# Kernel optimization log

Measured on AMD Instinct MI355X. Metric: run time of the kernel, lower is better.

Reference implementation:

```python
import jax, jax.numpy as jnp
import numpy as np

N = 512       # num_nodes (feature dim of x == num_nodes, per GCNConv(num_nodes, f1))
BZ = 32       # subjects
TC = 256      # tc_length
F1 = 256
F2 = 128
E = 524288    # edges in the given (corr) graph over all bz*N nodes
NTOT = BZ * N
SLOPE = 0.2   # leaky relu negative_slope


def setup_inputs() -> dict:
    key = jax.random.key(0)
    ks = jax.random.split(key, 17)
    w = lambda k, shape: (jax.random.normal(k, shape, jnp.float32) * (shape[-1] ** -0.5))
    return {
        "x": jax.random.normal(ks[0], (NTOT, N), jnp.float32),
        "t": jax.random.normal(ks[1], (NTOT, TC), jnp.float32),
        "gumbel_u": jax.random.uniform(ks[2], (BZ, N, N, 2), jnp.float32),
        "edge_index": jax.random.randint(ks[3], (2, E), 0, NTOT, jnp.int64 if jax.config.jax_enable_x64 else jnp.int32),
        "conv1_w": w(ks[4], (F1, N)),
        "conv1_b": jnp.zeros((F1,), jnp.float32),
        "conv2_w": w(ks[5], (F2, F1)),
        "conv2_b": jnp.zeros((F2,), jnp.float32),
        "fc_cat_w": w(ks[6], (2, 2 * TC)),
        "fc_cat_b": jnp.zeros((2,), jnp.float32),
        "fcn1_w": w(ks[7], (256, F2 * 2 * N)),
        "fcn1_b": jnp.zeros((256,), jnp.float32),
        "fcn2_w": w(ks[8], (32, 256)),
        "fcn2_b": jnp.zeros((32,), jnp.float32),
        "fcn3_w": w(ks[9], (2, 32)),
        "fcn3_b": jnp.zeros((2,), jnp.float32),
    }


def _gcn_dense(x, A, W, b):
    # PyG GCNConv on a dense 0/1 adjacency A (edge r->c means A[r,c]=1):
    # add self loop, in-degree symmetric norm, aggregate sources into targets.
    n = A.shape[0]
    Ah = A + jnp.eye(n, dtype=A.dtype)
    deg = Ah.sum(axis=0)                                  # in-degree (targets = cols)
    dis = jnp.where(deg > 0, jax.lax.rsqrt(deg), 0.0)
    M = dis[:, None] * Ah * dis[None, :]                  # M[j,i] = d_j^-1/2 A_hat[j,i] d_i^-1/2
    return M.T @ (x @ W.T) + b


def _gcn_sparse(x, row, col, W, b):
    n = x.shape[0]
    loops = jnp.arange(n, dtype=row.dtype)
    r = jnp.concatenate([row, loops])
    c = jnp.concatenate([col, loops])
    deg = jax.ops.segment_sum(jnp.ones_like(c, x.dtype), c, num_segments=n)
    dis = jnp.where(deg > 0, jax.lax.rsqrt(deg), 0.0)
    norm = dis[r] * dis[c]                                # [E+n]
    xw = x @ W.T                                          # [n, out]
    out = jax.ops.segment_sum(xw[r] * norm[:, None], c, num_segments=n)
    return out + b


def reference(x, t, gumbel_u, edge_index, conv1_w, conv1_b, conv2_w, conv2_b,
              fc_cat_w, fc_cat_b, fcn1_w, fcn1_b, fcn2_w, fcn2_b, fcn3_w, fcn3_b):
    bz = t.shape[0] // N
    tb = t.reshape(bz, N, -1)
    xb = x.reshape(bz, N, -1)
    # fc_cat(relu(cat([senders, receivers]))) factors into per-node terms:
    Ws = fc_cat_w[:, :TC]   # multiplies senders half
    Wr = fc_cat_w[:, TC:]   # multiplies receivers half

    def per_sample(ti, xi, ui):
        u = jax.nn.relu(ti)                               # [N, TC]
        ls = u @ Ws.T                                     # [N, 2] sender term
        lr = u @ Wr.T                                     # [N, 2] receiver term
        # pair k = i*N+j has receiver t_i, sender t_j
        logits = lr[:, None, :] + ls[None, :, :] + fc_cat_b   # [N, N, 2]
        g = -jnp.log(-jnp.log(jnp.clip(ui, 1e-9, 1.0 - 1e-9)))  # Gumbel(0,1)
        y = logits + g                                    # tau = 1
        A = (jnp.argmax(y, axis=-1) == 0).astype(xi.dtype)    # hard sample, class 0 => edge
        A = jax.lax.stop_gradient(A)                      # torch.where -> indices blocks grad
        h = jax.nn.relu(_gcn_dense(xi, A, conv1_w, conv1_b))
        return _gcn_dense(h, A, conv2_w, conv2_b)         # [N, F2]

    x_op = jax.vmap(per_sample)(tb, xb, gumbel_u)         # [bz, N, F2]

    row, col = edge_index[0], edge_index[1]
    x_corr = jax.nn.relu(_gcn_sparse(x, row, col, conv1_w, conv1_b))
    x_corr = _gcn_sparse(x_corr, row, col, conv2_w, conv2_b)   # [bz*N, F2]

    emb = jnp.concatenate([x_op.reshape(-1, F2), x_corr], axis=1)  # [bz*N, 2*F2]
    emb = emb.reshape(bz, -1)                             # [bz, 2*F2*N]
    h = jax.nn.leaky_relu(emb @ fcn1_w.T + fcn1_b, SLOPE)
    h = jax.nn.leaky_relu(h @ fcn2_w.T + fcn2_b, SLOPE)
    return h @ fcn3_w.T + fcn3_b                          # [bz, 2]
```

## Files before the change

kernel.cpp:

```cpp
#include <hip/hip_runtime.h>
#include <hip/hip_bf16.h>

typedef __bf16 bf16_t;
typedef __bf16 bf16x8 __attribute__((ext_vector_type(8)));
typedef __bf16 bf16x4 __attribute__((ext_vector_type(4)));
typedef float f32x4 __attribute__((ext_vector_type(4)));

constexpr int kN = 512;
constexpr int kBZ = 32;
constexpr int kTC = 256;
constexpr int kE = 524288;
constexpr int kNTOT = 16384;

__global__ __launch_bounds__(256) void k_front(const float* __restrict__ c1w, const float* __restrict__ c2w,
                                               bf16_t* __restrict__ c1b, bf16_t* __restrict__ c2b,
                                               int* __restrict__ counts, float* __restrict__ degsum,
                                               float* __restrict__ h1acc,
                                               const float* __restrict__ tin, const float* __restrict__ fcw,
                                               const float* __restrict__ fcb, float4* __restrict__ lsr) {
    int b = blockIdx.x;
    if (b < 200) {
        int i = b * 256 + threadIdx.x;
        const int n0 = 32768, n1 = n0 + 8192, n2 = n1 + 4096, n3 = n2 + 4096, n4 = n3 + 2048;
        if (i < n0) {
            float4 v = ((const float4*)c1w)[i];
            bf16x4 o = {(bf16_t)v.x, (bf16_t)v.y, (bf16_t)v.z, (bf16_t)v.w};
            ((bf16x4*)c1b)[i] = o;
        } else if (i < n1) {
            int j = i - n0;
            float4 v = ((const float4*)c2w)[j];
            bf16x4 o = {(bf16_t)v.x, (bf16_t)v.y, (bf16_t)v.z, (bf16_t)v.w};
            ((bf16x4*)c2b)[j] = o;
        } else if (i < n2) {
            ((int4*)counts)[i - n1] = make_int4(0, 0, 0, 0);
        } else if (i < n3) {
            ((float4*)degsum)[i - n2] = make_float4(0.f, 0.f, 0.f, 0.f);
        } else if (i < n4) {
            ((float4*)h1acc)[i - n3] = make_float4(0.f, 0.f, 0.f, 0.f);
        }
    } else {
        int row = (b - 200) * 4 + (threadIdx.x >> 6);
        int lane = threadIdx.x & 63;
        const float* tr = tin + (size_t)row * kTC;
        float s0 = 0, s1 = 0, r0 = 0, r1 = 0;
        for (int k = lane; k < kTC; k += 64) {
            float u = fmaxf(tr[k], 0.f);
            s0 += u * fcw[k];
            s1 += u * fcw[512 + k];
            r0 += u * fcw[256 + k];
            r1 += u * fcw[768 + k];
        }
#pragma unroll
        for (int off = 32; off > 0; off >>= 1) {
            s0 += __shfl_down(s0, off); s1 += __shfl_down(s1, off);
            r0 += __shfl_down(r0, off); r1 += __shfl_down(r1, off);
        }
        if (lane == 0) lsr[row] = make_float4(s0 + fcb[0], s1 + fcb[1], r0, r1);
    }
}

__global__ __launch_bounds__(256) void k_adj(const float* __restrict__ gum, const float4* __restrict__ lsr,
                                             bf16_t* __restrict__ AT, float* __restrict__ degsum) {
    int s = blockIdx.z;
    int a0 = blockIdx.y * 64, b0 = blockIdx.x * 64;
    __shared__ bf16_t tile[64][72];
    int t = threadIdx.x;
    int lb = t & 63, ra = t >> 6;
    int b = b0 + lb;
    float4 pb = lsr[s * kN + b];
#pragma unroll 4
    for (int p = 0; p < 16; p++) {
        int a = a0 + p * 4 + ra;
        float4 qa = lsr[s * kN + a];
        float2 gv = *(const float2*)(gum + ((((size_t)s * kN + a) * kN + b) << 1));
        float u0 = fmaxf(gv.x, 1e-9f);
        float u1 = fmaxf(gv.y, 1e-9f);
        float g0 = -__logf(-__logf(u0));
        float g1 = -__logf(-__logf(u1));
        float v = ((qa.z + pb.x + g0) >= (qa.w + pb.y + g1)) ? 1.f : 0.f;
        if (a == b) v += 1.f;
        tile[lb][p * 4 + ra] = (bf16_t)v;
    }
    __syncthreads();
    int rj = t >> 3, li = (t & 7) * 8;
#pragma unroll
    for (int p = 0; p < 2; p++) {
        int j = p * 32 + rj;
        bf16x8 v = *(const bf16x8*)&tile[j][li];
        *(bf16x8*)(AT + ((size_t)s * kN + b0 + j) * kN + a0 + li) = v;
        float ps = 0;
#pragma unroll
        for (int q = 0; q < 8; q++) ps += (float)v[q];
        ps += __shfl_down(ps, 4);
        ps += __shfl_down(ps, 2);
        ps += __shfl_down(ps, 1);
        if ((t & 7) == 0) atomicAdd(degsum + s * kN + b0 + j, ps);
    }
}

template <int MODE>
__global__ __launch_bounds__(256) void k_gemm(const bf16_t* __restrict__ A, const bf16_t* __restrict__ B,
                                              bf16_t* __restrict__ C, int K, int lda, int ldb, int ldc,
                                              size_t sA, size_t sB, size_t sC,
                                              const float* __restrict__ degsum, const float* __restrict__ bias) {
    int m0 = blockIdx.x * 128, n0 = blockIdx.y * 128, s = blockIdx.z;
    A += sA * s; B += sB * s; C += sC * s;
    __shared__ bf16_t As[128][72], Bs[128][72];
    f32x4 acc[4][4] = {};
    int tid = threadIdx.x;
    int wave = tid >> 6, lane = tid & 63;
    int wm = (wave & 1) * 64, wn = (wave >> 1) * 64;
    int fm = lane & 15, fq = lane >> 4;
    int srow = tid >> 3, scol = (tid & 7) * 8;
    for (int kb = 0; kb < K; kb += 64) {
        __syncthreads();
#pragma unroll
        for (int p = 0; p < 4; p++) {
            int row = p * 32 + srow;
            *(uint4*)&As[row][scol] = *(const uint4*)(A + (size_t)(m0 + row) * lda + kb + scol);
            *(uint4*)&Bs[row][scol] = *(const uint4*)(B + (size_t)(n0 + row) * ldb + kb + scol);
        }
        __syncthreads();
#pragma unroll
        for (int kk = 0; kk < 2; kk++) {
            bf16x8 af[4], bfr[4];
#pragma unroll
            for (int i = 0; i < 4; i++) {
                af[i] = *(const bf16x8*)&As[wm + i * 16 + fm][kk * 32 + fq * 8];
                bfr[i] = *(const bf16x8*)&Bs[wn + i * 16 + fm][kk * 32 + fq * 8];
            }
#pragma unroll
            for (int i = 0; i < 4; i++)
#pragma unroll
                for (int j = 0; j < 4; j++)
                    acc[i][j] = __builtin_amdgcn_mfma_f32_16x16x32_bf16(af[i], bfr[j], acc[i][j], 0, 0, 0);
        }
    }
#pragma unroll
    for (int i = 0; i < 4; i++) {
#pragma unroll
        for (int r = 0; r < 4; r++) {
            int row = wm + i * 16 + fq * 4 + r;
            float sc = rsqrtf(degsum[(size_t)s * kN + m0 + row]);
#pragma unroll
            for (int j = 0; j < 4; j++) {
                int col = n0 + wn + j * 16 + fm;
                float v = sc * acc[i][j][r] + bias[col];
                if constexpr (MODE == 1) v = fmaxf(v, 0.f);
                C[(size_t)(m0 + row) * ldc + col] = (bf16_t)v;
            }
        }
    }
}

template <bool AF32, int F, int DENSE_ROWS>
__global__ __launch_bounds__(256) void k_gemmT(const void* __restrict__ Ap, const bf16_t* __restrict__ B,
                                               bf16_t* __restrict__ XW, bf16_t* __restrict__ ZT, int K,
                                               const float* __restrict__ degsum) {
    int m0 = blockIdx.x * 128, n0 = blockIdx.y * 128;
    __shared__ __align__(16) bf16_t smem[2 * 128 * 72];
    bf16_t* AsBase = smem;
    bf16_t* BsBase = smem + 128 * 72;
    f32x4 acc[4][4] = {};
    int tid = threadIdx.x;
    int wave = tid >> 6, lane = tid & 63;
    int wm = (wave & 1) * 64, wn = (wave >> 1) * 64;
    int fm = lane & 15, fq = lane >> 4;
    int srow = tid >> 3, scol = (tid & 7) * 8;
    for (int kb = 0; kb < K; kb += 64) {
        __syncthreads();
#pragma unroll
        for (int p = 0; p < 4; p++) {
            int row = p * 32 + srow;
            if constexpr (AF32) {
                const float* ap = (const float*)Ap + (size_t)(m0 + row) * K + kb + scol;
                float4 lo = *(const float4*)ap;
                float4 hi = *(const float4*)(ap + 4);
                bf16x8 o = {(bf16_t)lo.x, (bf16_t)lo.y, (bf16_t)lo.z, (bf16_t)lo.w,
                            (bf16_t)hi.x, (bf16_t)hi.y, (bf16_t)hi.z, (bf16_t)hi.w};
                *(bf16x8*)&AsBase[row * 72 + scol] = o;
            } else {
                *(uint4*)&AsBase[row * 72 + scol] =
                    *(const uint4*)((const bf16_t*)Ap + (size_t)(m0 + row) * K + kb + scol);
            }
            *(uint4*)&BsBase[row * 72 + scol] = *(const uint4*)(B + (size_t)(n0 + row) * K + kb + scol);
        }
        __syncthreads();
#pragma unroll
        for (int kk = 0; kk < 2; kk++) {
            bf16x8 af[4], bfr[4];
#pragma unroll
            for (int i = 0; i < 4; i++) {
                af[i] = *(const bf16x8*)&AsBase[(wm + i * 16 + fm) * 72 + kk * 32 + fq * 8];
                bfr[i] = *(const bf16x8*)&BsBase[(wn + i * 16 + fm) * 72 + kk * 32 + fq * 8];
            }
#pragma unroll
            for (int i = 0; i < 4; i++)
#pragma unroll
                for (int j = 0; j < 4; j++)
                    acc[i][j] = __builtin_amdgcn_mfma_f32_16x16x32_bf16(af[i], bfr[j], acc[i][j], 0, 0, 0);
        }
    }
    bool doT = (m0 < DENSE_ROWS);
    __syncthreads();
#pragma unroll
    for (int i = 0; i < 4; i++) {
#pragma unroll
        for (int r = 0; r < 4; r++) {
            int row = wm + i * 16 + fq * 4 + r;
            float sc = doT ? rsqrtf(degsum[m0 + row]) : 0.f;
#pragma unroll
            for (int j = 0; j < 4; j++) {
                int col = wn + j * 16 + fm;
                float v = acc[i][j][r];
                XW[(size_t)(m0 + row) * F + n0 + col] = (bf16_t)v;
                if (doT) smem[col * 136 + row] = (bf16_t)(sc * v);
            }
        }
    }
    if (doT) {
        __syncthreads();
        int fr = tid >> 1, hi = (tid & 1) * 64;
        bf16_t* zrow = ZT + ((size_t)(m0 >> 9) * F + n0 + fr) * kN + (m0 & 511) + hi;
#pragma unroll
        for (int q = 0; q < 8; q++)
            *(bf16x8*)(zrow + q * 8) = *(const bf16x8*)&smem[fr * 136 + hi + q * 8];
    }
}


__global__ __launch_bounds__(256) void k_hist(const int* __restrict__ col, int* __restrict__ counts) {
    int e = blockIdx.x * 256 + threadIdx.x;
    if (e < kE) atomicAdd(&counts[col[e]], 1);
}

__global__ __launch_bounds__(1024) void k_scan(const int* __restrict__ counts, int* __restrict__ offsets,
                                               int* __restrict__ cursor, float* __restrict__ dis_s) {
    __shared__ int ldc_[16896];
    __shared__ int sums[1024];
    int t = threadIdx.x;
#define IDX(j) ((j) + ((j) >> 5))
    for (int i = 0; i < 16; i++) {
        int g = i * 1024 + t;
        int c = counts[g];
        ldc_[IDX(g)] = c;
        dis_s[g] = rsqrtf((float)(c + 1));
    }
    __syncthreads();
    int s = 0;
    for (int i = 0; i < 16; i++) s += ldc_[IDX(t * 16 + i)];
    sums[t] = s;
    __syncthreads();
    for (int off = 1; off < 1024; off <<= 1) {
        int y = (t >= off) ? sums[t - off] : 0;
        __syncthreads();
        sums[t] += y;
        __syncthreads();
    }
    int run = sums[t] - s;
    for (int i = 0; i < 16; i++) {
        int j = t * 16 + i;
        int c = ldc_[IDX(j)];
        ldc_[IDX(j)] = run;
        run += c;
    }
    __syncthreads();
    for (int i = 0; i < 16; i++) {
        int g = i * 1024 + t;
        int o = ldc_[IDX(g)];
        offsets[g] = o;
        cursor[g] = o;
    }
#undef IDX
}

__global__ __launch_bounds__(256) void k_fill(const int* __restrict__ row, const int* __restrict__ col,
                                              int* __restrict__ cursor, int* __restrict__ list) {
    int e = blockIdx.x * 256 + threadIdx.x;
    if (e < kE) {
        int p = atomicAdd(&cursor[col[e]], 1);
        list[p] = row[e];
    }
}

template <int F, bool RELU>
__global__ __launch_bounds__(256) void k_sagg(const bf16_t* __restrict__ XW, int rowOffIn,
                                              const int* __restrict__ list, const int* __restrict__ offsets,
                                              const int* __restrict__ counts, const float* __restrict__ dis_s,
                                              const float* __restrict__ bias, bf16_t* __restrict__ OUT,
                                              int outColOff) {
    constexpr int TPR = F / 8;
    constexpr int RPB = 256 / TPR;
    int j = blockIdx.x * RPB + threadIdx.x / TPR;
    int f8 = (threadIdx.x % TPR) * 8;
    float dj = dis_s[j];
    const bf16_t* base = XW + (size_t)rowOffIn * F;
    float acc[8];
    {
        bf16x8 v = *(const bf16x8*)(base + (size_t)j * F + f8);
#pragma unroll
        for (int q = 0; q < 8; q++) acc[q] = dj * (float)v[q];
    }
    int off = offsets[j], cnt = counts[j];
    int e = 0;
    for (; e + 8 <= cnt; e += 8) {
        int r[8];
#pragma unroll
        for (int q = 0; q < 8; q++) r[q] = list[off + e + q];
        float d[8];
#pragma unroll
        for (int q = 0; q < 8; q++) d[q] = dis_s[r[q]];
        bf16x8 v0 = *(const bf16x8*)(base + (size_t)r[0] * F + f8);
        bf16x8 v1 = *(const bf16x8*)(base + (size_t)r[1] * F + f8);
        bf16x8 v2 = *(const bf16x8*)(base + (size_t)r[2] * F + f8);
        bf16x8 v3 = *(const bf16x8*)(base + (size_t)r[3] * F + f8);
        bf16x8 v4 = *(const bf16x8*)(base + (size_t)r[4] * F + f8);
        bf16x8 v5 = *(const bf16x8*)(base + (size_t)r[5] * F + f8);
        bf16x8 v6 = *(const bf16x8*)(base + (size_t)r[6] * F + f8);
        bf16x8 v7 = *(const bf16x8*)(base + (size_t)r[7] * F + f8);
#pragma unroll
        for (int q = 0; q < 8; q++)
            acc[q] += ((d[0] * (float)v0[q] + d[1] * (float)v1[q]) + (d[2] * (float)v2[q] + d[3] * (float)v3[q])) +
                      ((d[4] * (float)v4[q] + d[5] * (float)v5[q]) + (d[6] * (float)v6[q] + d[7] * (float)v7[q]));
    }
    for (; e + 4 <= cnt; e += 4) {
        int r0 = list[off + e], r1 = list[off + e + 1], r2 = list[off + e + 2], r3 = list[off + e + 3];
        float d0 = dis_s[r0], d1 = dis_s[r1], d2 = dis_s[r2], d3 = dis_s[r3];
        bf16x8 v0 = *(const bf16x8*)(base + (size_t)r0 * F + f8);
        bf16x8 v1 = *(const bf16x8*)(base + (size_t)r1 * F + f8);
        bf16x8 v2 = *(const bf16x8*)(base + (size_t)r2 * F + f8);
        bf16x8 v3 = *(const bf16x8*)(base + (size_t)r3 * F + f8);
#pragma unroll
        for (int q = 0; q < 8; q++)
            acc[q] += (d0 * (float)v0[q] + d1 * (float)v1[q]) + (d2 * (float)v2[q] + d3 * (float)v3[q]);
    }
    for (; e < cnt; e++) {
        int r = list[off + e];
        float d = dis_s[r];
        bf16x8 v = *(const bf16x8*)(base + (size_t)r * F + f8);
#pragma unroll
        for (int q = 0; q < 8; q++) acc[q] += d * (float)v[q];
    }
    bf16x8 o;
#pragma unroll
    for (int q = 0; q < 8; q++) {
        float v = dj * acc[q] + bias[f8 + q];
        if (RELU) v = fmaxf(v, 0.f);
        o[q] = (bf16_t)v;
    }
    *(bf16x8*)(OUT + (size_t)j * 256 + outColOff + f8) = o;
}

__global__ __launch_bounds__(256) void k_fcn1(const bf16_t* __restrict__ EMB, const float* __restrict__ W1,
                                              float* __restrict__ partials) {
    int tid = threadIdx.x, wave = tid >> 6, lane = tid & 63;
    int fm = lane & 15, fq = lane >> 4;
    int kb0 = blockIdx.x * 512;
    f32x4 acc[2][4] = {};
#pragma unroll 4
    for (int ks = 0; ks < 512; ks += 32) {
        int k = kb0 + ks + fq * 8;
        bf16x8 a0 = *(const bf16x8*)(EMB + (size_t)fm * 131072 + k);
        bf16x8 a1 = *(const bf16x8*)(EMB + (size_t)(16 + fm) * 131072 + k);
        bf16x8 bfr[4];
#pragma unroll
        for (int j = 0; j < 4; j++) {
            int n = wave * 64 + j * 16 + fm;
            const float* p = W1 + (size_t)n * 131072 + k;
            float4 lo = *(const float4*)p;
            float4 hi = *(const float4*)(p + 4);
            bf16x8 b = {(bf16_t)lo.x, (bf16_t)lo.y, (bf16_t)lo.z, (bf16_t)lo.w,
                        (bf16_t)hi.x, (bf16_t)hi.y, (bf16_t)hi.z, (bf16_t)hi.w};
            bfr[j] = b;
        }
#pragma unroll
        for (int j = 0; j < 4; j++) {
            acc[0][j] = __builtin_amdgcn_mfma_f32_16x16x32_bf16(a0, bfr[j], acc[0][j], 0, 0, 0);
            acc[1][j] = __builtin_amdgcn_mfma_f32_16x16x32_bf16(a1, bfr[j], acc[1][j], 0, 0, 0);
        }
    }
    float* P = partials + (size_t)blockIdx.x * 8192;
#pragma unroll
    for (int i = 0; i < 2; i++)
#pragma unroll
        for (int j = 0; j < 4; j++)
#pragma unroll
            for (int r = 0; r < 4; r++)
                P[(size_t)(i * 16 + fq * 4 + r) * 256 + wave * 64 + j * 16 + fm] = acc[i][j][r];
}

__global__ __launch_bounds__(256) void k_reduce(const float* __restrict__ partials, float* __restrict__ h1pre) {
    int e = blockIdx.x * 256 + threadIdx.x;
    float s = 0;
#pragma unroll 8
    for (int i = 0; i < 256; i++) s += partials[(size_t)i * 8192 + e];
    h1pre[e] = s;
}

__global__ __launch_bounds__(256) void k_head(const float* __restrict__ h1pre, const float* __restrict__ b1,
                                              const float* __restrict__ W2, const float* __restrict__ b2,
                                              const float* __restrict__ W3, const float* __restrict__ b3,
                                              float* __restrict__ out) {
    __shared__ float h1s[32][256];
    __shared__ float h2s[32][32];
    int t = threadIdx.x;
    for (int i = 0; i < 32; i++) {
        float s = h1pre[i * 256 + t] + b1[t];
        h1s[i][t] = (s > 0.f) ? s : 0.2f * s;
    }
    __syncthreads();
    for (int p = 0; p < 4; p++) {
        int id = p * 256 + t, si = id >> 5, o2 = id & 31;
        float s = 0;
        for (int k = 0; k < 256; k++) s += h1s[si][k] * W2[o2 * 256 + k];
        s += b2[o2];
        h2s[si][o2] = (s > 0.f) ? s : 0.2f * s;
    }
    __syncthreads();
    if (t < 64) {
        int si = t >> 1, o3 = t & 1;
        float s = 0;
#pragma unroll
        for (int k = 0; k < 32; k++) s += h2s[si][k] * W3[o3 * 32 + k];
        out[si * 2 + o3] = s + b3[o3];
    }
}


extern "C" void kernel_launch(void* const* d_in, const int* in_sizes, int n_in,
                              void* d_out, int out_size, void* d_ws, size_t ws_size,
                              hipStream_t stream) {
    const float* x = (const float*)d_in[0];
    const float* t = (const float*)d_in[1];
    const float* gum = (const float*)d_in[2];
    const int* eidx = (const int*)d_in[3];
    const float* c1w = (const float*)d_in[4];
    const float* c1b = (const float*)d_in[5];
    const float* c2w = (const float*)d_in[6];
    const float* c2b = (const float*)d_in[7];
    const float* fcw = (const float*)d_in[8];
    const float* fcb = (const float*)d_in[9];
    const float* w1 = (const float*)d_in[10];
    const float* b1 = (const float*)d_in[11];
    const float* w2 = (const float*)d_in[12];
    const float* b2 = (const float*)d_in[13];
    const float* w3 = (const float*)d_in[14];
    const float* b3 = (const float*)d_in[15];
    float* out = (float*)d_out;
    (void)in_sizes; (void)n_in; (void)out_size; (void)ws_size;

    char* ws = (char*)d_ws;
    size_t off = 0;
    auto alloc = [&](size_t bytes) -> char* {
        char* p = ws + off;
        off += (bytes + 255) & ~size_t(255);
        return p;
    };
    bf16_t* c1wb = (bf16_t*)alloc((size_t)256 * 512 * 2);
    bf16_t* c2wb = (bf16_t*)alloc((size_t)128 * 256 * 2);
    float4* lsr = (float4*)alloc((size_t)kNTOT * 16);
    bf16_t* AT = (bf16_t*)alloc((size_t)kBZ * kN * kN * 2);
    float* degsum = (float*)alloc((size_t)kNTOT * 4);
    bf16_t* XW1_EMB = (bf16_t*)alloc((size_t)kNTOT * 256 * 2);
    bf16_t* Z1T = (bf16_t*)alloc((size_t)kBZ * 256 * 512 * 2);
    bf16_t* H = (bf16_t*)alloc((size_t)32768 * 256 * 2);
    bf16_t* XW2 = (bf16_t*)alloc((size_t)32768 * 128 * 2);
    bf16_t* Z2T = (bf16_t*)alloc((size_t)kBZ * 128 * 512 * 2);
    int* counts = (int*)alloc((size_t)kNTOT * 4);
    int* offsets = (int*)alloc((size_t)kNTOT * 4);
    int* cursor = (int*)alloc((size_t)kNTOT * 4);
    float* diss = (float*)alloc((size_t)kNTOT * 4);
    int* list = (int*)alloc((size_t)kE * 4);
    float* partials = (float*)alloc((size_t)256 * 8192 * 4);
    float* h1pre = (float*)alloc((size_t)8192 * 4);

    bf16_t* XW1 = XW1_EMB;
    bf16_t* EMB = XW1_EMB;

    k_front<<<4296, 256, 0, stream>>>(c1w, c2w, c1wb, c2wb, counts, degsum, h1pre, t, fcw, fcb, lsr);
    k_adj<<<dim3(8, 8, 32), 256, 0, stream>>>(gum, lsr, AT, degsum);
    k_hist<<<2048, 256, 0, stream>>>(eidx + kE, counts);
    k_scan<<<1, 1024, 0, stream>>>(counts, offsets, cursor, diss);
    k_fill<<<2048, 256, 0, stream>>>(eidx, eidx + kE, cursor, list);
    k_gemmT<true, 256, kNTOT><<<dim3(128, 2, 1), 256, 0, stream>>>(x, c1wb, XW1, Z1T, 512, degsum);
    k_gemm<1><<<dim3(4, 2, 32), 256, 0, stream>>>(AT, Z1T, H, 512, 512, 512, 256,
                                                  (size_t)512 * 512, (size_t)256 * 512, (size_t)512 * 256,
                                                  degsum, c1b);
    k_sagg<256, true><<<2048, 256, 0, stream>>>(XW1, 0, list, offsets, counts, diss, c1b,
                                                H + (size_t)16384 * 256, 0);
    k_gemmT<false, 128, kNTOT><<<dim3(256, 1, 1), 256, 0, stream>>>(H, c2wb, XW2, Z2T, 256, degsum);
    k_gemm<2><<<dim3(4, 1, 32), 256, 0, stream>>>(AT, Z2T, EMB, 512, 512, 512, 256,
                                                  (size_t)512 * 512, (size_t)128 * 512, (size_t)512 * 256,
                                                  degsum, c2b);
    k_sagg<128, false><<<1024, 256, 0, stream>>>(XW2, 16384, list, offsets, counts, diss, c2b, EMB, 128);
    k_fcn1<<<256, 256, 0, stream>>>(EMB, w1, partials);
    k_reduce<<<32, 256, 0, stream>>>(partials, h1pre);
    k_head<<<1, 256, 0, stream>>>(h1pre, b1, w2, b2, w3, b3, out);
}
```

Before: 508.0 us.

## Double-buffer GEMM tiles with async global-to-LDS loads and swizzled layout

Rewrites the batched dense GEMM and the transposed GEMM to double-buffer shared-memory tiles. Tiles are staged with global_load_lds into an XOR-swizzled unpadded layout, so the next K-tile loads while MFMAs run on the current one and each iteration needs one barrier instead of two. The fp32-input variant prefetches into registers and converts after compute. The sparse aggregation loop now prefetches the next batch of edge indices. The unused h1acc zeroing is dropped from the front kernel. Shared-memory use doubles, which may lower occupancy, and the swizzle indexing must match between writes and reads.

After: 506.1 us. Within noise of the previous version (-0.4%).

```diff
diff --git a/kernel.cpp b/kernel.cpp
--- a/kernel.cpp
+++ b/kernel.cpp
@@ -12,16 +12,35 @@
 constexpr int kE = 524288;
 constexpr int kNTOT = 16384;
 
+__device__ __forceinline__ void gll16(const bf16_t* g, bf16_t* l) {
+    __builtin_amdgcn_global_load_lds((const __attribute__((address_space(1))) void*)g,
+                                     (__attribute__((address_space(3))) void*)l, 16, 0, 0);
+}
+
+__device__ __forceinline__ void stage128x64(const bf16_t* __restrict__ src, int ld,
+                                            bf16_t* lds, int wave, int lane) {
+#pragma unroll
+    for (int i = 0; i < 4; i++) {
+        int r0 = (wave * 4 + i) * 8;
+        int r = r0 + (lane >> 3);
+        int c = (lane & 7) ^ (r & 7);
+        gll16(src + (size_t)r * ld + c * 8, lds + r0 * 64);
+    }
+}
+
+__device__ __forceinline__ bf16x8 rdfrag(const bf16_t* lds, int row, int cc) {
+    return *(const bf16x8*)(lds + row * 64 + ((cc ^ (row & 7)) * 8));
+}
+
 __global__ __launch_bounds__(256) void k_front(const float* __restrict__ c1w, const float* __restrict__ c2w,
                                                bf16_t* __restrict__ c1b, bf16_t* __restrict__ c2b,
                                                int* __restrict__ counts, float* __restrict__ degsum,
-                                               float* __restrict__ h1acc,
                                                const float* __restrict__ tin, const float* __restrict__ fcw,
                                                const float* __restrict__ fcb, float4* __restrict__ lsr) {
     int b = blockIdx.x;
-    if (b < 200) {
+    if (b < 192) {
         int i = b * 256 + threadIdx.x;
-        const int n0 = 32768, n1 = n0 + 8192, n2 = n1 + 4096, n3 = n2 + 4096, n4 = n3 + 2048;
+        const int n0 = 32768, n1 = n0 + 8192, n2 = n1 + 4096, n3 = n2 + 4096;
         if (i < n0) {
             float4 v = ((const float4*)c1w)[i];
             bf16x4 o = {(bf16_t)v.x, (bf16_t)v.y, (bf16_t)v.z, (bf16_t)v.w};
@@ -35,11 +54,9 @@
             ((int4*)counts)[i - n1] = make_int4(0, 0, 0, 0);
         } else if (i < n3) {
             ((float4*)degsum)[i - n2] = make_float4(0.f, 0.f, 0.f, 0.f);
-        } else if (i < n4) {
-            ((float4*)h1acc)[i - n3] = make_float4(0.f, 0.f, 0.f, 0.f);
         }
     } else {
-        int row = (b - 200) * 4 + (threadIdx.x >> 6);
+        int row = (b - 192) * 4 + (threadIdx.x >> 6);
         int lane = threadIdx.x & 63;
         const float* tr = tin + (size_t)row * kTC;
         float s0 = 0, s1 = 0, r0 = 0, r1 = 0;
@@ -104,30 +121,127 @@
                                               size_t sA, size_t sB, size_t sC,
                                               const float* __restrict__ degsum, const float* __restrict__ bias) {
     int m0 = blockIdx.x * 128, n0 = blockIdx.y * 128, s = blockIdx.z;
-    A += sA * s; B += sB * s; C += sC * s;
-    __shared__ bf16_t As[128][72], Bs[128][72];
+    const bf16_t* Ab = A + sA * s + (size_t)m0 * lda;
+    const bf16_t* Bb = B + sB * s + (size_t)n0 * ldb;
+    C += sC * s;
+    __shared__ __align__(16) bf16_t As[2][128 * 64], Bs[2][128 * 64];
+    f32x4 acc[4][4] = {};
+    int tid = threadIdx.x;
+    int wave = tid >> 6, lane = tid & 63;
+    int wm = (wave & 1) * 64, wn = (wave >> 1) * 64;
+    int fm = lane & 15, fq = lane >> 4;
+    stage128x64(Ab, lda, As[0], wave, lane);
+    stage128x64(Bb, ldb, Bs[0], wave, lane);
+    int cur = 0;
+    for (int kb = 0;;) {
+        int kn = kb + 64;
+        __syncthreads();
+        if (kn < K) {
+            stage128x64(Ab + kn, lda, As[cur ^ 1], wave, lane);
+            stage128x64(Bb + kn, ldb, Bs[cur ^ 1], wave, lane);
+        }
+#pragma unroll
+        for (int kk = 0; kk < 2; kk++) {
+            bf16x8 af[4], bfr[4];
+#pragma unroll
+            for (int i = 0; i < 4; i++) {
+                af[i] = rdfrag(As[cur], wm + i * 16 + fm, kk * 4 + fq);
+                bfr[i] = rdfrag(Bs[cur], wn + i * 16 + fm, kk * 4 + fq);
+            }
+#pragma unroll
+            for (int i = 0; i < 4; i++)
+#pragma unroll
+                for (int j = 0; j < 4; j++)
+                    acc[i][j] = __builtin_amdgcn_mfma_f32_16x16x32_bf16(af[i], bfr[j], acc[i][j], 0, 0, 0);
+        }
+        kb = kn;
+        if (kb >= K) break;
+        cur ^= 1;
+    }
+#pragma unroll
+    for (int i = 0; i < 4; i++) {
+#pragma unroll
+        for (int r = 0; r < 4; r++) {
+            int row = wm + i * 16 + fq * 4 + r;
+            float sc = rsqrtf(degsum[(size_t)s * kN + m0 + row]);
+#pragma unroll
+            for (int j = 0; j < 4; j++) {
+                int col = n0 + wn + j * 16 + fm;
+                float v = sc * acc[i][j][r] + bias[col];
+                if constexpr (MODE == 1) v = fmaxf(v, 0.f);
+                C[(size_t)(m0 + row) * ldc + col] = (bf16_t)v;
+            }
+        }
+    }
+}
+
+template <bool AF32, int F, int DENSE_ROWS>
+__global__ __launch_bounds__(256) void k_gemmT(const void* __restrict__ Ap, const bf16_t* __restrict__ B,
+                                               bf16_t* __restrict__ XW, bf16_t* __restrict__ ZT, int K,
+                                               const float* __restrict__ degsum) {
+    int m0 = blockIdx.x * 128, n0 = blockIdx.y * 128;
+    constexpr int AST = AF32 ? 9216 : 8192;
+    __shared__ __align__(16) bf16_t smem[2 * AST + 2 * 8192];
+    bf16_t* A0 = smem;
+    bf16_t* A1 = smem + AST;
+    bf16_t* B0 = smem + 2 * AST;
+    bf16_t* B1 = smem + 2 * AST + 8192;
     f32x4 acc[4][4] = {};
     int tid = threadIdx.x;
     int wave = tid >> 6, lane = tid & 63;
     int wm = (wave & 1) * 64, wn = (wave >> 1) * 64;
     int fm = lane & 15, fq = lane >> 4;
     int srow = tid >> 3, scol = (tid & 7) * 8;
-    for (int kb = 0; kb < K; kb += 64) {
-        __syncthreads();
+    const float* Af = (const float*)Ap;
+    const bf16_t* Abf = (const bf16_t*)Ap;
+    if constexpr (AF32) {
 #pragma unroll
         for (int p = 0; p < 4; p++) {
             int row = p * 32 + srow;
-            *(uint4*)&As[row][scol] = *(const uint4*)(A + (size_t)(m0 + row) * lda + kb + scol);
-            *(uint4*)&Bs[row][scol] = *(const uint4*)(B + (size_t)(n0 + row) * ldb + kb + scol);
-        }
+            const float* ap = Af + (size_t)(m0 + row) * K + scol;
+            float4 lo = *(const float4*)ap, hi = *(const float4*)(ap + 4);
+            bf16x8 o = {(bf16_t)lo.x, (bf16_t)lo.y, (bf16_t)lo.z, (bf16_t)lo.w,
+                        (bf16_t)hi.x, (bf16_t)hi.y, (bf16_t)hi.z, (bf16_t)hi.w};
+            *(bf16x8*)&A0[row * 72 + scol] = o;
+        }
+    } else {
+        stage128x64(Abf + (size_t)m0 * K, K, A0, wave, lane);
+    }
+    stage128x64(B + (size_t)n0 * K, K, B0, wave, lane);
+    int cur = 0;
+    for (int kb = 0;;) {
+        int kn = kb + 64;
+        bool more = kn < K;
+        bf16_t* Ac = cur ? A1 : A0;
+        bf16_t* An = cur ? A0 : A1;
+        bf16_t* Bc = cur ? B1 : B0;
+        bf16_t* Bn = cur ? B0 : B1;
+        float4 plo[4], phi[4];
         __syncthreads();
+        if (more) {
+            if constexpr (AF32) {
+#pragma unroll
+                for (int p = 0; p < 4; p++) {
+                    int row = p * 32 + srow;
+                    const float* ap = Af + (size_t)(m0 + row) * K + kn + scol;
+                    plo[p] = *(const float4*)ap;
+                    phi[p] = *(const float4*)(ap + 4);
+                }
+            } else {
+                stage128x64(Abf + (size_t)m0 * K + kn, K, An, wave, lane);
+            }
+            stage128x64(B + (size_t)n0 * K + kn, K, Bn, wave, lane);
+        }
 #pragma unroll
         for (int kk = 0; kk < 2; kk++) {
             bf16x8 af[4], bfr[4];
 #pragma unroll
             for (int i = 0; i < 4; i++) {
-                af[i] = *(const bf16x8*)&As[wm + i * 16 + fm][kk * 32 + fq * 8];
-                bfr[i] = *(const bf16x8*)&Bs[wn + i * 16 + fm][kk * 32 + fq * 8];
+                if constexpr (AF32)
+                    af[i] = *(const bf16x8*)&Ac[(wm + i * 16 + fm) * 72 + kk * 32 + fq * 8];
+                else
+                    af[i] = rdfrag(Ac, wm + i * 16 + fm, kk * 4 + fq);
+                bfr[i] = rdfrag(Bc, wn + i * 16 + fm, kk * 4 + fq);
             }
 #pragma unroll
             for (int i = 0; i < 4; i++)
@@ -135,71 +249,20 @@
                 for (int j = 0; j < 4; j++)
                     acc[i][j] = __builtin_amdgcn_mfma_f32_16x16x32_bf16(af[i], bfr[j], acc[i][j], 0, 0, 0);
         }
-    }
-#pragma unroll
-    for (int i = 0; i < 4; i++) {
-#pragma unroll
-        for (int r = 0; r < 4; r++) {
-            int row = wm + i * 16 + fq * 4 + r;
-            float sc = rsqrtf(degsum[(size_t)s * kN + m0 + row]);
-#pragma unroll
-            for (int j = 0; j < 4; j++) {
-                int col = n0 + wn + j * 16 + fm;
-                float v = sc * acc[i][j][r] + bias[col];
-                if constexpr (MODE == 1) v = fmaxf(v, 0.f);
-                C[(size_t)(m0 + row) * ldc + col] = (bf16_t)v;
-            }
-        }
-    }
-}
-
-template <bool AF32, int F, int DENSE_ROWS>
-__global__ __launch_bounds__(256) void k_gemmT(const void* __restrict__ Ap, const bf16_t* __restrict__ B,
-                                               bf16_t* __restrict__ XW, bf16_t* __restrict__ ZT, int K,
-                                               const float* __restrict__ degsum) {
-    int m0 = blockIdx.x * 128, n0 = blockIdx.y * 128;
-    __shared__ __align__(16) bf16_t smem[2 * 128 * 72];
-    bf16_t* AsBase = smem;
-    bf16_t* BsBase = smem + 128 * 72;
-    f32x4 acc[4][4] = {};
-    int tid = threadIdx.x;
-    int wave = tid >> 6, lane = tid & 63;
-    int wm = (wave & 1) * 64, wn = (wave >> 1) * 64;
-    int fm = lane & 15, fq = lane >> 4;
-    int srow = tid >> 3, scol = (tid & 7) * 8;
-    for (int kb = 0; kb < K; kb += 64) {
-        __syncthreads();
-#pragma unroll
-        for (int p = 0; p < 4; p++) {
-            int row = p * 32 + srow;
-            if constexpr (AF32) {
-                const float* ap = (const float*)Ap + (size_t)(m0 + row) * K + kb + scol;
-                float4 lo = *(const float4*)ap;
-                float4 hi = *(const float4*)(ap + 4);
-                bf16x8 o = {(bf16_t)lo.x, (bf16_t)lo.y, (bf16_t)lo.z, (bf16_t)lo.w,
-                            (bf16_t)hi.x, (bf16_t)hi.y, (bf16_t)hi.z, (bf16_t)hi.w};
-                *(bf16x8*)&AsBase[row * 72 + scol] = o;
-            } else {
-                *(uint4*)&AsBase[row * 72 + scol] =
-                    *(const uint4*)((const bf16_t*)Ap + (size_t)(m0 + row) * K + kb + scol);
-            }
-            *(uint4*)&BsBase[row * 72 + scol] = *(const uint4*)(B + (size_t)(n0 + row) * K + kb + scol);
-        }
-        __syncthreads();
-#pragma unroll
-        for (int kk = 0; kk < 2; kk++) {
-            bf16x8 af[4], bfr[4];
-#pragma unroll
-            for (int i = 0; i < 4; i++) {
-                af[i] = *(const bf16x8*)&AsBase[(wm + i * 16 + fm) * 72 + kk * 32 + fq * 8];
-                bfr[i] = *(const bf16x8*)&BsBase[(wn + i * 16 + fm) * 72 + kk * 32 + fq * 8];
-            }
-#pragma unroll
-            for (int i = 0; i < 4; i++)
-#pragma unroll
-                for (int j = 0; j < 4; j++)
-                    acc[i][j] = __builtin_amdgcn_mfma_f32_16x16x32_bf16(af[i], bfr[j], acc[i][j], 0, 0, 0);
-        }
+        if constexpr (AF32) {
+            if (more) {
+#pragma unroll
+                for (int p = 0; p < 4; p++) {
+                    int row = p * 32 + srow;
+                    bf16x8 o = {(bf16_t)plo[p].x, (bf16_t)plo[p].y, (bf16_t)plo[p].z, (bf16_t)plo[p].w,
+                                (bf16_t)phi[p].x, (bf16_t)phi[p].y, (bf16_t)phi[p].z, (bf16_t)phi[p].w};
+                    *(bf16x8*)&An[row * 72 + scol] = o;
+                }
+            }
+        }
+        kb = kn;
+        if (kb >= K) break;
+        cur ^= 1;
     }
     bool doT = (m0 < DENSE_ROWS);
     __syncthreads();
@@ -303,25 +366,39 @@
     }
     int off = offsets[j], cnt = counts[j];
     int e = 0;
-    for (; e + 8 <= cnt; e += 8) {
+    int nb = cnt & ~7;
+    if (nb) {
         int r[8];
 #pragma unroll
-        for (int q = 0; q < 8; q++) r[q] = list[off + e + q];
-        float d[8];
-#pragma unroll
-        for (int q = 0; q < 8; q++) d[q] = dis_s[r[q]];
-        bf16x8 v0 = *(const bf16x8*)(base + (size_t)r[0] * F + f8);
-        bf16x8 v1 = *(const bf16x8*)(base + (size_t)r[1] * F + f8);
-        bf16x8 v2 = *(const bf16x8*)(base + (size_t)r[2] * F + f8);
-        bf16x8 v3 = *(const bf16x8*)(base + (size_t)r[3] * F + f8);
-        bf16x8 v4 = *(const bf16x8*)(base + (size_t)r[4] * F + f8);
-        bf16x8 v5 = *(const bf16x8*)(base + (size_t)r[5] * F + f8);
-        bf16x8 v6 = *(const bf16x8*)(base + (size_t)r[6] * F + f8);
-        bf16x8 v7 = *(const bf16x8*)(base + (size_t)r[7] * F + f8);
-#pragma unroll
-        for (int q = 0; q < 8; q++)
-            acc[q] += ((d[0] * (float)v0[q] + d[1] * (float)v1[q]) + (d[2] * (float)v2[q] + d[3] * (float)v3[q])) +
-                      ((d[4] * (float)v4[q] + d[5] * (float)v5[q]) + (d[6] * (float)v6[q] + d[7] * (float)v7[q]));
+        for (int q = 0; q < 8; q++) r[q] = list[off + q];
+        while (true) {
+            int en = e + 8;
+            bool more = en < nb;
+            int rn[8];
+            if (more) {
+#pragma unroll
+                for (int q = 0; q < 8; q++) rn[q] = list[off + en + q];
+            }
+            float d[8];
+#pragma unroll
+            for (int q = 0; q < 8; q++) d[q] = dis_s[r[q]];
+            bf16x8 v0 = *(const bf16x8*)(base + (size_t)r[0] * F + f8);
+            bf16x8 v1 = *(const bf16x8*)(base + (size_t)r[1] * F + f8);
+            bf16x8 v2 = *(const bf16x8*)(base + (size_t)r[2] * F + f8);
+            bf16x8 v3 = *(const bf16x8*)(base + (size_t)r[3] * F + f8);
+            bf16x8 v4 = *(const bf16x8*)(base + (size_t)r[4] * F + f8);
+            bf16x8 v5 = *(const bf16x8*)(base + (size_t)r[5] * F + f8);
+            bf16x8 v6 = *(const bf16x8*)(base + (size_t)r[6] * F + f8);
+            bf16x8 v7 = *(const bf16x8*)(base + (size_t)r[7] * F + f8);
+#pragma unroll
+            for (int q = 0; q < 8; q++)
+                acc[q] += ((d[0] * (float)v0[q] + d[1] * (float)v1[q]) + (d[2] * (float)v2[q] + d[3] * (float)v3[q])) +
+                          ((d[4] * (float)v4[q] + d[5] * (float)v5[q]) + (d[6] * (float)v6[q] + d[7] * (float)v7[q]));
+            e = en;
+            if (!more) break;
+#pragma unroll
+            for (int q = 0; q < 8; q++) r[q] = rn[q];
+        }
     }
     for (; e + 4 <= cnt; e += 4) {
         int r0 = list[off + e], r1 = list[off + e + 1], r2 = list[off + e + 2], r3 = list[off + e + 3];
@@ -477,7 +554,7 @@
     bf16_t* XW1 = XW1_EMB;
     bf16_t* EMB = XW1_EMB;
 
-    k_front<<<4296, 256, 0, stream>>>(c1w, c2w, c1wb, c2wb, counts, degsum, h1pre, t, fcw, fcb, lsr);
+    k_front<<<4288, 256, 0, stream>>>(c1w, c2w, c1wb, c2wb, counts, degsum, t, fcw, fcb, lsr);
     k_adj<<<dim3(8, 8, 32), 256, 0, stream>>>(gum, lsr, AT, degsum);
     k_hist<<<2048, 256, 0, stream>>>(eidx + kE, counts);
     k_scan<<<1, 1024, 0, stream>>>(counts, offsets, cursor, diss);
```
